# Kernel tuning notes

Hardware: AMD Instinct MI355X
Metric: run time of the kernel (lower is better)

Reference implementation:

```python
import jax, jax.numpy as jnp
import numpy as np

D_MODEL = 1024
NHEAD = 16
D_K = D_MODEL // NHEAD


def setup_inputs() -> dict:
    key = jax.random.key(0)
    ks = jax.random.split(key, 10)
    B, S = 2, 2048
    x = jax.random.normal(ks[0], (B, S, D_MODEL), dtype=jnp.float32)
    # sorted 1-D coordinate grid in [0,1], shape [S,1,1] so coords.shape[1]==1
    coords = jnp.sort(jax.random.uniform(ks[1], (S, 1, 1), dtype=jnp.float32), axis=0)
    sc = 1.0 / np.sqrt(D_MODEL)
    Wq = jax.random.normal(ks[2], (D_MODEL, D_MODEL), dtype=jnp.float32) * sc
    bq = jnp.zeros((D_MODEL,), jnp.float32)
    Wk = jax.random.normal(ks[3], (D_MODEL, D_MODEL), dtype=jnp.float32) * sc
    bk = jnp.zeros((D_MODEL,), jnp.float32)
    Wv = jax.random.normal(ks[4], (D_MODEL, D_MODEL), dtype=jnp.float32) * sc
    bv = jnp.zeros((D_MODEL,), jnp.float32)
    Wo = jax.random.normal(ks[5], (D_MODEL, D_MODEL), dtype=jnp.float32) * sc
    bo = jnp.zeros((D_MODEL,), jnp.float32)
    return {"x": x, "coords": coords, "Wq": Wq, "bq": bq, "Wk": Wk, "bk": bk,
            "Wv": Wv, "bv": bv, "Wo": Wo, "bo": bo}


def _split_heads(t):  # [B,S,D] -> [B,H,S,Dk]
    B, S, _ = t.shape
    return t.reshape(B, S, NHEAD, D_K).transpose(0, 2, 1, 3)


def reference(x, coords, Wq, bq, Wk, bk, Wv, bv, Wo, bo):
    B, S, _ = x.shape
    Q = _split_heads(x @ Wq.T + bq)
    K = _split_heads(x @ Wk.T + bk)
    V = _split_heads(x @ Wv.T + bv)

    scale = jnp.sqrt(jnp.float32(D_K))
    scores = jnp.einsum('bhld,bhsd->bhls', Q, K) / scale  # [B,H,S,S]

    # trapezoidal quadrature weights from coord grid: [S-1] -> broadcast shapes
    dc = jnp.abs(coords[1:] - coords[:-1]).reshape(1, 1, 1, S - 1)  # key-axis

    # custom trapezoidal softmax
    e = jnp.exp(scores - jnp.max(scores, axis=-1, keepdims=True))
    denom = jnp.sum(0.5 * dc * (e[..., 1:] + e[..., :-1]), axis=-1, keepdims=True)
    aw = e / denom  # [B,H,S,S]

    dcv = dc.reshape(1, 1, S - 1, 1)  # value-axis weighting
    o1 = jnp.einsum('bhls,bhsd->bhld', aw[..., 1:], dcv * V[:, :, 1:, :])
    o2 = jnp.einsum('bhls,bhsd->bhld', aw[..., :-1], dcv * V[:, :, :-1, :])
    out = 0.5 * (o1 + o2)  # [B,H,S,Dk]

    out = out.transpose(0, 2, 1, 3).reshape(B, S, D_MODEL)
    return out @ Wo.T + bo
```

## Files before the change

kernel.cpp:

```cpp
#include <hip/hip_runtime.h>

#define DM 1024
#define NHEAD 16
#define DK 64
#define QLD 3072

typedef short bf16x8 __attribute__((ext_vector_type(8)));
typedef float f32x4 __attribute__((ext_vector_type(4)));

__device__ __forceinline__ unsigned short f2bf(float f) {
  union { float f; unsigned u; } v; v.f = f;
  return (unsigned short)((v.u + 0x7fffu + ((v.u >> 16) & 1u)) >> 16);
}
__device__ __forceinline__ float bf2f(unsigned short h) {
  union { unsigned u; float f; } v; v.u = ((unsigned)h) << 16; return v.f;
}
__device__ __forceinline__ float fexp2(float x) {
  float r; asm("v_exp_f32 %0, %1" : "=v"(r) : "v"(x)); return r;
}

__device__ __forceinline__ void gld16(const void* g, void* l) {
  __builtin_amdgcn_global_load_lds((const __attribute__((address_space(1))) void*)g,
                                   (__attribute__((address_space(3))) void*)l, 16, 0, 0);
}

__device__ __forceinline__ int kappa(int p) {
  return (p & 32) + (((p & 7) >> 2) << 4) + (((p >> 3) & 3) << 2) + (p & 3);
}

__global__ void k_prep(const float* __restrict__ x, const float* __restrict__ Wq,
                       const float* __restrict__ Wk, const float* __restrict__ Wv,
                       const float* __restrict__ Wo, const float* __restrict__ bq,
                       const float* __restrict__ bk, const float* __restrict__ bv,
                       const float* __restrict__ coords,
                       unsigned short* __restrict__ xb, unsigned short* __restrict__ Wcat,
                       unsigned short* __restrict__ Wob, float* __restrict__ bcat,
                       float* __restrict__ tw, unsigned short* __restrict__ twb,
                       int M, int S, float QS) {
  const int nx = M * DM / 4;
  const int nw = DM * DM / 4;
  const int total = nx + 4 * nw;
  int gid = blockIdx.x * 256 + threadIdx.x;

  auto conv4 = [&](const float* src, unsigned short* dst, int idx, float sc) {
    float4 v = *(const float4*)(src + idx * 4);
    ushort4 o;
    o.x = f2bf(v.x * sc); o.y = f2bf(v.y * sc);
    o.z = f2bf(v.z * sc); o.w = f2bf(v.w * sc);
    *(ushort4*)(dst + idx * 4) = o;
  };

  if (gid < nx) { conv4(x, xb, gid, 1.0f); return; }
  if (gid < nx + nw) { conv4(Wq, Wcat, gid - nx, QS); return; }
  if (gid < nx + 2 * nw) { conv4(Wk, Wcat + DM * DM, gid - nx - nw, 1.0f); return; }
  if (gid < nx + 3 * nw) { conv4(Wv, Wcat + 2 * DM * DM, gid - nx - 2 * nw, 1.0f); return; }
  if (gid < total) { conv4(Wo, Wob, gid - nx - 3 * nw, 1.0f); return; }

  int r = gid - total;
  if (r < 3 * DM) {
    float v = (r < DM) ? bq[r] * QS : (r < 2 * DM ? bk[r - DM] : bv[r - 2 * DM]);
    bcat[r] = v;
    return;
  }
  r -= 3 * DM;
  if (r < S) {
    auto twval = [&](int k) {
      float a = (k > 0)     ? fabsf(coords[k] - coords[k - 1]) : 0.f;
      float b = (k < S - 1) ? fabsf(coords[k + 1] - coords[k]) : 0.f;
      return 0.5f * (a + b);
    };
    tw[r] = twval(r);
    int key = (r & ~63) + kappa(r & 63);
    twb[r] = f2bf(twval(key));
  }
}

#define BM 128
#define BN 128
#define BKK 64

template<int VFUSE>
__global__ __launch_bounds__(256)
void gemm_bt(const unsigned short* __restrict__ A, const unsigned short* __restrict__ B,
             const float* __restrict__ bias, void* __restrict__ C,
             int M, int N, int K, int ldc,
             const float* __restrict__ twp, unsigned short* __restrict__ Vt, int S) {
  __shared__ __align__(16) unsigned short smem[4][BM * BKK];
  const int tid = threadIdx.x;
  const int lane = tid & 63;
  const int wid = tid >> 6;
  const int rr = lane & 15, g = lane >> 4;
  const int nbn = N / BN;
  const int cpx = gridDim.x >> 3;
  const int bid = ((gridDim.x & 7) == 0) ? (blockIdx.x & 7) * cpx + (blockIdx.x >> 3)
                                         : blockIdx.x;
  const int bm = bid / nbn, bn = bid % nbn;
  const int wr = wid >> 1, wc = wid & 1;
  const int nkt = K / BKK;

  const unsigned short* Abase = A + (size_t)bm * BM * K;
  const unsigned short* Bbase = B + (size_t)bn * BN * K;

  auto stage = [&](int buf, int kt) {
#pragma unroll
    for (int j = 0; j < 4; ++j) {
      int o = j * 256 + tid;
      int row = o >> 3;
      int cb = ((o & 7) * 16) ^ ((row & 7) << 4);
      gld16((const char*)(Abase + (size_t)row * K + kt * BKK) + cb, &smem[buf][o * 8]);
      gld16((const char*)(Bbase + (size_t)row * K + kt * BKK) + cb, &smem[2 + buf][o * 8]);
    }
  };

  f32x4 acc[4][4] = {};
  stage(0, 0);
  int cur = 0;
  const int sw = (rr & 7) << 4;
  for (int kt = 0; kt < nkt; ++kt) {
    __syncthreads();
    if (kt + 1 < nkt) stage(cur ^ 1, kt + 1);
    const char* a0 = (const char*)&smem[cur][0];
    const char* b0 = (const char*)&smem[2 + cur][0];
#pragma unroll
    for (int kk = 0; kk < 2; ++kk) {
      const int co = (kk * 64 + g * 16);
      bf16x8 af[4], bfr[4];
#pragma unroll
      for (int m = 0; m < 4; ++m)
        af[m] = *(const bf16x8*)(a0 + (wr * 64 + m * 16 + rr) * 128 + (co ^ sw));
#pragma unroll
      for (int n = 0; n < 4; ++n)
        bfr[n] = *(const bf16x8*)(b0 + (wc * 64 + n * 16 + rr) * 128 + (co ^ sw));
      __builtin_amdgcn_s_setprio(1);
#pragma unroll
      for (int m = 0; m < 4; ++m)
#pragma unroll
        for (int n = 0; n < 4; ++n)
          acc[m][n] = __builtin_amdgcn_mfma_f32_16x16x32_bf16(af[m], bfr[n], acc[m][n], 0, 0, 0);
      __builtin_amdgcn_s_setprio(0);
    }
    cur ^= 1;
  }

  const int ccol0 = bn * BN + wc * 64;
  unsigned short* L = &smem[0][0];
  __syncthreads();
#pragma unroll
  for (int n = 0; n < 4; ++n) {
    const float bn_ = bias ? bias[ccol0 + n * 16 + rr] : 0.f;
#pragma unroll
    for (int m = 0; m < 4; ++m)
#pragma unroll
      for (int r = 0; r < 4; ++r)
        L[(wr * 64 + m * 16 + g * 4 + r) * 136 + wc * 64 + n * 16 + rr] =
            f2bf(acc[m][n][r] + bn_);
  }
  __syncthreads();
  if (VFUSE && bn >= (2 * DM) / BN) {
    const int tilesPerB = S / BM;
    const int bb = bm / tilesPerB;
    const int s0 = (bm % tilesPerB) * BM;
    const int vcol0 = bn * BN - 2 * DM;
    const int hh = tid >> 7;
    const int dd = (tid >> 1) & 63;
    const int stl = tid & 1;
    const int head = (vcol0 >> 6) + hh;
    const int lcol = hh * 64 + dd;
    unsigned short* vdst = Vt + ((size_t)(bb * NHEAD + head) * DK + dd) * S + s0 + stl * 64;
    const float* twg = twp + s0 + stl * 64;
    unsigned short tmp[8];
#pragma unroll
    for (int j8 = 0; j8 < 8; ++j8) {
#pragma unroll
      for (int j = 0; j < 8; ++j) {
        const int kl = kappa(j8 * 8 + j);
        tmp[j] = f2bf(bf2f(L[(stl * 64 + kl) * 136 + lcol]) * twg[kl]);
      }
      *(uint4*)&vdst[j8 * 8] = *(const uint4*)&tmp[0];
    }
  } else {
    unsigned short* Cb = (unsigned short*)C + (size_t)(bm * BM) * ldc + bn * BN;
#pragma unroll
    for (int i = 0; i < 8; ++i) {
      int o = i * 256 + tid;
      int row = o >> 4;
      int cc = (o & 15) * 8;
      uint4 v = *(const uint4*)&L[row * 136 + cc];
      *(uint4*)&Cb[(size_t)row * ldc + cc] = v;
    }
  }
}

#define WBM 64
__global__ __launch_bounds__(256)
void gemm_wo(const unsigned short* __restrict__ A, const unsigned short* __restrict__ B,
             const float* __restrict__ bias, float* __restrict__ C,
             int M, int N, int K, int ldc) {
  __shared__ __align__(16) unsigned short smem[6][WBM * BKK];
  const int tid = threadIdx.x;
  const int lane = tid & 63;
  const int wid = tid >> 6;
  const int rr = lane & 15, g = lane >> 4;
  const int nbn = N / BN;
  const int cpx = gridDim.x >> 3;
  const int bid = (blockIdx.x & 7) * cpx + (blockIdx.x >> 3);
  const int bm = bid / nbn, bn = bid % nbn;
  const int wr = wid >> 1, wc = wid & 1;
  const int nkt = K / BKK;

  const unsigned short* Abase = A + (size_t)bm * WBM * K;
  const unsigned short* Bbase = B + (size_t)bn * BN * K;

  auto stage = [&](int buf, int kt) {
    {
#pragma unroll
      for (int j = 0; j < 2; ++j) {
        int o = j * 256 + tid;
        int row = o >> 3;
        int cb = ((o & 7) * 16) ^ ((row & 7) << 4);
        gld16((const char*)(Abase + (size_t)row * K + kt * BKK) + cb, &smem[buf][o * 8]);
      }
    }
    {
#pragma unroll
      for (int j = 0; j < 4; ++j) {
        int o = j * 256 + tid;
        int row = o >> 3;
        int cb = ((o & 7) * 16) ^ ((row & 7) << 4);
        gld16((const char*)(Bbase + (size_t)row * K + kt * BKK) + cb, &smem[2 + buf * 2][o * 8]);
      }
    }
  };

  f32x4 acc[2][4] = {};
  stage(0, 0);
  int cur = 0;
  const int sw = (rr & 7) << 4;
  for (int kt = 0; kt < nkt; ++kt) {
    __syncthreads();
    if (kt + 1 < nkt) stage(cur ^ 1, kt + 1);
    const char* a0 = (const char*)&smem[cur][0];
    const char* b0 = (const char*)&smem[2 + cur * 2][0];
#pragma unroll
    for (int kk = 0; kk < 2; ++kk) {
      const int co = (kk * 64 + g * 16);
      bf16x8 af[2], bfr[4];
#pragma unroll
      for (int m = 0; m < 2; ++m)
        af[m] = *(const bf16x8*)(a0 + (wr * 32 + m * 16 + rr) * 128 + (co ^ sw));
#pragma unroll
      for (int n = 0; n < 4; ++n)
        bfr[n] = *(const bf16x8*)(b0 + (wc * 64 + n * 16 + rr) * 128 + (co ^ sw));
      __builtin_amdgcn_s_setprio(1);
#pragma unroll
      for (int m = 0; m < 2; ++m)
#pragma unroll
        for (int n = 0; n < 4; ++n)
          acc[m][n] = __builtin_amdgcn_mfma_f32_16x16x32_bf16(af[m], bfr[n], acc[m][n], 0, 0, 0);
      __builtin_amdgcn_s_setprio(0);
    }
    cur ^= 1;
  }

  float* Lf = (float*)&smem[0][0];
  __syncthreads();
#pragma unroll
  for (int n = 0; n < 4; ++n) {
    const float bn_ = bias[bn * BN + wc * 64 + n * 16 + rr];
#pragma unroll
    for (int m = 0; m < 2; ++m)
#pragma unroll
      for (int r = 0; r < 4; ++r)
        Lf[(wr * 32 + m * 16 + g * 4 + r) * 132 + wc * 64 + n * 16 + rr] =
            acc[m][n][r] + bn_;
  }
  __syncthreads();
  float* Cb = C + (size_t)(bm * WBM) * ldc + bn * BN;
#pragma unroll
  for (int i = 0; i < 8; ++i) {
    int o = i * 256 + tid;
    int row = o >> 5;
    int cc = (o & 31) * 4;
    float4 v = *(const float4*)&Lf[row * 132 + cc];
    *(float4*)&Cb[(size_t)row * ldc + cc] = v;
  }
}

__global__ __launch_bounds__(256)
void k_attn(const unsigned short* __restrict__ QKV, const unsigned short* __restrict__ Vt,
            const unsigned short* __restrict__ twb, unsigned short* __restrict__ O, int S) {
  __shared__ __align__(16) unsigned short sK[2][128 * 64];
  __shared__ __align__(16) unsigned short sV[2][2][64 * 64];
  const int tid = threadIdx.x, lane = tid & 63, wid = tid >> 6;
  const int rr = lane & 15, g = lane >> 4;
  const int nqt = S / 128;
  const int cpx = gridDim.x >> 3;
  const int swz = (blockIdx.x & 7) * cpx + (blockIdx.x >> 3);
  const int qt = swz % nqt;
  const int bh = swz / nqt;
  const int h = bh & (NHEAD - 1), b = bh / NHEAD;

  const unsigned short* Qbase = QKV + ((size_t)b * S + qt * 128 + wid * 32) * QLD + h * DK;
  const unsigned short* Kbase = QKV + (size_t)b * S * QLD + DM + h * DK;
  const unsigned short* Vbase = Vt + (size_t)bh * DK * S;

  bf16x8 aq[2][2];
#pragma unroll
  for (int qm = 0; qm < 2; ++qm) {
    aq[qm][0] = *(const bf16x8*)&Qbase[(size_t)(qm * 16 + rr) * QLD + g * 8];
    aq[qm][1] = *(const bf16x8*)&Qbase[(size_t)(qm * 16 + rr) * QLD + 32 + g * 8];
  }

  f32x4 acc[2][5] = {};
  const f32x4 z0 = {};

  auto stage = [&](int buf, int kt) {
#pragma unroll
    for (int j = 0; j < 4; ++j) {
      int o = j * 256 + tid;
      int row = o >> 3;
      int cb = ((o & 7) * 16) ^ ((row & 7) << 4);
      gld16((const char*)(Kbase + (size_t)(kt * 128 + row) * QLD) + cb, &sK[buf][o * 8]);
    }
#pragma unroll
    for (int j = 0; j < 4; ++j) {
      int o = j * 256 + tid;
      int half_ = o >> 9;
      int r = o & 511;
      int row = r >> 3;
      int cb = ((r & 7) * 16) ^ ((row & 7) << 4);
      gld16((const char*)(Vbase + (size_t)row * S + kt * 128 + half_ * 64) + cb,
            &sV[buf][0][o * 8]);
    }
  };

  stage(0, 0);
  int cur = 0;
  const int nkt = S / 128;
  const int swr = (rr & 7) << 4;
  for (int kt = 0; kt < nkt; ++kt) {
    __syncthreads();
    if (kt + 1 < nkt) stage(cur ^ 1, kt + 1);

#pragma unroll
    for (int half = 0; half < 2; ++half) {
      bf16x8 kA[4][2];
#pragma unroll
      for (int f = 0; f < 4; ++f) {
        const int row = half * 64 + f * 16 + rr;
        kA[f][0] = *(const bf16x8*)((const char*)&sK[cur][row * 64] + ((g * 16) ^ swr));
        kA[f][1] = *(const bf16x8*)((const char*)&sK[cur][row * 64] + ((64 + g * 16) ^ swr));
      }
      bf16x8 vB[2][4];
#pragma unroll
      for (int kk = 0; kk < 2; ++kk)
#pragma unroll
        for (int n = 0; n < 4; ++n) {
          const int vrow = n * 16 + rr;
          const int cb = (kk * 64 + g * 16) ^ ((vrow & 7) << 4);
          vB[kk][n] = *(const bf16x8*)((const char*)&sV[cur][half][vrow * 64] + cb);
        }
      bf16x8 tw0 = *(const bf16x8*)&twb[kt * 128 + half * 64 + g * 8];
      bf16x8 tw1 = *(const bf16x8*)&twb[kt * 128 + half * 64 + 32 + g * 8];

      f32x4 s[2][4];
      __builtin_amdgcn_s_setprio(1);
#pragma unroll
      for (int f = 0; f < 4; ++f)
#pragma unroll
        for (int qm = 0; qm < 2; ++qm) {
          f32x4 z = __builtin_amdgcn_mfma_f32_16x16x32_bf16(kA[f][0], aq[qm][0], z0, 0, 0, 0);
          s[qm][f] = __builtin_amdgcn_mfma_f32_16x16x32_bf16(kA[f][1], aq[qm][1], z, 0, 0, 0);
        }
      __builtin_amdgcn_s_setprio(0);

#pragma unroll
      for (int qm = 0; qm < 2; ++qm)
#pragma unroll
        for (int f = 0; f < 4; ++f)
#pragma unroll
          for (int r = 0; r < 4; ++r)
            s[qm][f][r] = fexp2(s[qm][f][r]);

      bf16x8 pa[2][2];
#pragma unroll
      for (int qm = 0; qm < 2; ++qm)
#pragma unroll
        for (int kk = 0; kk < 2; ++kk) {
          union { bf16x8 v; unsigned u[4]; } pk;
          asm("v_cvt_pk_bf16_f32 %0, %1, %2" : "=v"(pk.u[0]) : "v"(s[qm][2*kk][0]),   "v"(s[qm][2*kk][1]));
          asm("v_cvt_pk_bf16_f32 %0, %1, %2" : "=v"(pk.u[1]) : "v"(s[qm][2*kk][2]),   "v"(s[qm][2*kk][3]));
          asm("v_cvt_pk_bf16_f32 %0, %1, %2" : "=v"(pk.u[2]) : "v"(s[qm][2*kk+1][0]), "v"(s[qm][2*kk+1][1]));
          asm("v_cvt_pk_bf16_f32 %0, %1, %2" : "=v"(pk.u[3]) : "v"(s[qm][2*kk+1][2]), "v"(s[qm][2*kk+1][3]));
          pa[qm][kk] = pk.v;
        }

      __builtin_amdgcn_s_setprio(1);
#pragma unroll
      for (int kk = 0; kk < 2; ++kk) {
#pragma unroll
        for (int n = 0; n < 4; ++n)
#pragma unroll
          for (int qm = 0; qm < 2; ++qm)
            acc[qm][n] = __builtin_amdgcn_mfma_f32_16x16x32_bf16(pa[qm][kk], vB[kk][n], acc[qm][n], 0, 0, 0);
#pragma unroll
        for (int qm = 0; qm < 2; ++qm)
          acc[qm][4] = __builtin_amdgcn_mfma_f32_16x16x32_bf16(pa[qm][kk], kk ? tw1 : tw0, acc[qm][4], 0, 0, 0);
      }
      __builtin_amdgcn_s_setprio(0);
    }
    cur ^= 1;
  }

  unsigned short* L = &sK[0][0];
  __syncthreads();
#pragma unroll
  for (int qm = 0; qm < 2; ++qm)
#pragma unroll
    for (int n = 0; n < 4; ++n)
#pragma unroll
      for (int r = 0; r < 4; ++r)
        L[(wid * 32 + qm * 16 + g * 4 + r) * 72 + n * 16 + rr] =
            f2bf(acc[qm][n][r] / acc[qm][4][r]);
  __syncthreads();
  unsigned short* Ob = O + ((size_t)b * S + qt * 128) * DM + h * DK;
#pragma unroll
  for (int i = 0; i < 4; ++i) {
    int o = i * 256 + tid;
    int row = o >> 3;
    int c = (o & 7) * 8;
    uint4 v = *(const uint4*)&L[row * 72 + c];
    *(uint4*)&Ob[(size_t)row * DM + c] = v;
  }
}

extern "C" void kernel_launch(void* const* d_in, const int* in_sizes, int n_in,
                              void* d_out, int out_size, void* d_ws, size_t ws_size,
                              hipStream_t stream) {
  const float* x      = (const float*)d_in[0];
  const float* coords = (const float*)d_in[1];
  const float* Wq = (const float*)d_in[2];
  const float* bq = (const float*)d_in[3];
  const float* Wk = (const float*)d_in[4];
  const float* bk = (const float*)d_in[5];
  const float* Wv = (const float*)d_in[6];
  const float* bv = (const float*)d_in[7];
  const float* Wo = (const float*)d_in[8];
  const float* bo = (const float*)d_in[9];

  const int S = in_sizes[1];
  const int B = in_sizes[0] / (S * DM);
  const int M = B * S;
  const float QS = 0.18033688011112042f;

  char* w = (char*)d_ws;
  size_t off = 0;
  unsigned short* xb   = (unsigned short*)(w + off); off += (size_t)M * DM * 2;
  unsigned short* Wcat = (unsigned short*)(w + off); off += (size_t)3 * DM * DM * 2;
  unsigned short* Wob  = (unsigned short*)(w + off); off += (size_t)DM * DM * 2;
  unsigned short* QKVb = (unsigned short*)(w + off); off += (size_t)M * QLD * 2;
  unsigned short* Vtb  = (unsigned short*)(w + off); off += (size_t)M * DM * 2;
  float* tw  = (float*)(w + off); off += (size_t)S * 4;
  unsigned short* twb = (unsigned short*)(w + off); off += (size_t)S * 2;
  float* bcat = (float*)(w + off); off += (size_t)3 * DM * 4;
  unsigned short* Ob = xb;
  (void)ws_size; (void)n_in; (void)out_size;

  {
    int nx = M * DM / 4, nw = DM * DM / 4;
    int total = nx + 4 * nw;
    int tail = 3 * DM + S;
    int gridp = total / 256 + (tail + 255) / 256;
    k_prep<<<gridp, 256, 0, stream>>>(x, Wq, Wk, Wv, Wo, bq, bk, bv, coords,
                                      xb, Wcat, Wob, bcat, tw, twb, M, S, QS);
  }

  gemm_bt<1><<<(M / BM) * (3 * DM / BN), 256, 0, stream>>>(
      xb, Wcat, bcat, QKVb, M, 3 * DM, DM, QLD, tw, Vtb, S);

  k_attn<<<B * NHEAD * (S / 128), 256, 0, stream>>>(QKVb, Vtb, twb, Ob, S);

  gemm_wo<<<(M / WBM) * (DM / BN), 256, 0, stream>>>(Ob, Wob, bo, (float*)d_out, M, DM, DM, DM);
}
```

Measured before the change: 107.3 us.

## Fuse fp32-to-bf16 weight conversion into GEMM B-tile staging

Weight conversion to bf16 is removed from the prep kernel. Instead each GEMM block loads fp32 weight tiles into registers, prefetching one k-step ahead, then converts and writes them to swizzled LDS after the MFMA loop. This saves a full pass that reads the weights and writes a bf16 copy. In exchange, every M-tile re-reads the fp32 weights at twice the bytes, register pressure rises, and a launch_bounds occupancy hint of 2 is added.

New measurement: 147.5 us. 37.6% more time.

```diff
diff --git a/kernel.cpp b/kernel.cpp
--- a/kernel.cpp
+++ b/kernel.cpp
@@ -24,39 +24,35 @@
                                    (__attribute__((address_space(3))) void*)l, 16, 0, 0);
 }
 
+__device__ __forceinline__ uint4 pack8(float4 a, float4 b, float sc) {
+  uint4 r;
+  r.x = (unsigned)f2bf(a.x * sc) | ((unsigned)f2bf(a.y * sc) << 16);
+  r.y = (unsigned)f2bf(a.z * sc) | ((unsigned)f2bf(a.w * sc) << 16);
+  r.z = (unsigned)f2bf(b.x * sc) | ((unsigned)f2bf(b.y * sc) << 16);
+  r.w = (unsigned)f2bf(b.z * sc) | ((unsigned)f2bf(b.w * sc) << 16);
+  return r;
+}
+
 __device__ __forceinline__ int kappa(int p) {
   return (p & 32) + (((p & 7) >> 2) << 4) + (((p >> 3) & 3) << 2) + (p & 3);
 }
 
-__global__ void k_prep(const float* __restrict__ x, const float* __restrict__ Wq,
-                       const float* __restrict__ Wk, const float* __restrict__ Wv,
-                       const float* __restrict__ Wo, const float* __restrict__ bq,
+__global__ void k_prep(const float* __restrict__ x, const float* __restrict__ bq,
                        const float* __restrict__ bk, const float* __restrict__ bv,
                        const float* __restrict__ coords,
-                       unsigned short* __restrict__ xb, unsigned short* __restrict__ Wcat,
-                       unsigned short* __restrict__ Wob, float* __restrict__ bcat,
+                       unsigned short* __restrict__ xb, float* __restrict__ bcat,
                        float* __restrict__ tw, unsigned short* __restrict__ twb,
                        int M, int S, float QS) {
-  const int nx = M * DM / 4;
-  const int nw = DM * DM / 4;
-  const int total = nx + 4 * nw;
+  const int nx8 = M * DM / 8;
   int gid = blockIdx.x * 256 + threadIdx.x;
 
-  auto conv4 = [&](const float* src, unsigned short* dst, int idx, float sc) {
-    float4 v = *(const float4*)(src + idx * 4);
-    ushort4 o;
-    o.x = f2bf(v.x * sc); o.y = f2bf(v.y * sc);
-    o.z = f2bf(v.z * sc); o.w = f2bf(v.w * sc);
-    *(ushort4*)(dst + idx * 4) = o;
-  };
-
-  if (gid < nx) { conv4(x, xb, gid, 1.0f); return; }
-  if (gid < nx + nw) { conv4(Wq, Wcat, gid - nx, QS); return; }
-  if (gid < nx + 2 * nw) { conv4(Wk, Wcat + DM * DM, gid - nx - nw, 1.0f); return; }
-  if (gid < nx + 3 * nw) { conv4(Wv, Wcat + 2 * DM * DM, gid - nx - 2 * nw, 1.0f); return; }
-  if (gid < total) { conv4(Wo, Wob, gid - nx - 3 * nw, 1.0f); return; }
-
-  int r = gid - total;
+  if (gid < nx8) {
+    float4 a = *(const float4*)(x + gid * 8);
+    float4 b = *(const float4*)(x + gid * 8 + 4);
+    *(uint4*)(xb + gid * 8) = pack8(a, b, 1.0f);
+    return;
+  }
+  int r = gid - nx8;
   if (r < 3 * DM) {
     float v = (r < DM) ? bq[r] * QS : (r < 2 * DM ? bk[r - DM] : bv[r - 2 * DM]);
     bcat[r] = v;
@@ -79,9 +75,10 @@
 #define BN 128
 #define BKK 64
 
-template<int VFUSE>
-__global__ __launch_bounds__(256)
-void gemm_bt(const unsigned short* __restrict__ A, const unsigned short* __restrict__ B,
+__global__ __launch_bounds__(256, 2)
+void gemm_bt(const unsigned short* __restrict__ A,
+             const float* __restrict__ Wq, const float* __restrict__ Wk,
+             const float* __restrict__ Wv, float QS,
              const float* __restrict__ bias, void* __restrict__ C,
              int M, int N, int K, int ldc,
              const float* __restrict__ twp, unsigned short* __restrict__ Vt, int S) {
@@ -92,33 +89,58 @@
   const int rr = lane & 15, g = lane >> 4;
   const int nbn = N / BN;
   const int cpx = gridDim.x >> 3;
-  const int bid = ((gridDim.x & 7) == 0) ? (blockIdx.x & 7) * cpx + (blockIdx.x >> 3)
-                                         : blockIdx.x;
+  const int bid = (blockIdx.x & 7) * cpx + (blockIdx.x >> 3);
   const int bm = bid / nbn, bn = bid % nbn;
   const int wr = wid >> 1, wc = wid & 1;
   const int nkt = K / BKK;
 
   const unsigned short* Abase = A + (size_t)bm * BM * K;
-  const unsigned short* Bbase = B + (size_t)bn * BN * K;
-
-  auto stage = [&](int buf, int kt) {
+  const int sel = bn >> 3;
+  const float* Wsel = (sel == 0) ? Wq : ((sel == 1) ? Wk : Wv);
+  const float wsc = (sel == 0) ? QS : 1.0f;
+  const int brow0 = bn * BN - sel * 1024;
+
+  auto stageA = [&](int buf, int kt) {
 #pragma unroll
     for (int j = 0; j < 4; ++j) {
       int o = j * 256 + tid;
       int row = o >> 3;
       int cb = ((o & 7) * 16) ^ ((row & 7) << 4);
       gld16((const char*)(Abase + (size_t)row * K + kt * BKK) + cb, &smem[buf][o * 8]);
-      gld16((const char*)(Bbase + (size_t)row * K + kt * BKK) + cb, &smem[2 + buf][o * 8]);
+    }
+  };
+
+  float4 vb0[4], vb1[4];
+  auto issueB = [&](int kt) {
+#pragma unroll
+    for (int j = 0; j < 4; ++j) {
+      int o = j * 256 + tid;
+      int row = o >> 3;
+      int ce = (o & 7) * 8;
+      const float* src = Wsel + (size_t)(brow0 + row) * K + kt * BKK + ce;
+      vb0[j] = *(const float4*)src;
+      vb1[j] = *(const float4*)(src + 4);
+    }
+  };
+  auto writeB = [&](int buf) {
+#pragma unroll
+    for (int j = 0; j < 4; ++j) {
+      int o = j * 256 + tid;
+      int row = o >> 3;
+      int cb = ((o & 7) * 16) ^ ((row & 7) << 4);
+      *(uint4*)((char*)&smem[2 + buf][0] + row * 128 + cb) = pack8(vb0[j], vb1[j], wsc);
     }
   };
 
   f32x4 acc[4][4] = {};
-  stage(0, 0);
+  stageA(0, 0);
+  issueB(0);
+  writeB(0);
   int cur = 0;
   const int sw = (rr & 7) << 4;
   for (int kt = 0; kt < nkt; ++kt) {
     __syncthreads();
-    if (kt + 1 < nkt) stage(cur ^ 1, kt + 1);
+    if (kt + 1 < nkt) { stageA(cur ^ 1, kt + 1); issueB(kt + 1); }
     const char* a0 = (const char*)&smem[cur][0];
     const char* b0 = (const char*)&smem[2 + cur][0];
 #pragma unroll
@@ -139,6 +161,7 @@
           acc[m][n] = __builtin_amdgcn_mfma_f32_16x16x32_bf16(af[m], bfr[n], acc[m][n], 0, 0, 0);
       __builtin_amdgcn_s_setprio(0);
     }
+    if (kt + 1 < nkt) writeB(cur ^ 1);
     cur ^= 1;
   }
 
@@ -156,7 +179,7 @@
             f2bf(acc[m][n][r] + bn_);
   }
   __syncthreads();
-  if (VFUSE && bn >= (2 * DM) / BN) {
+  if (bn >= (2 * DM) / BN) {
     const int tilesPerB = S / BM;
     const int bb = bm / tilesPerB;
     const int s0 = (bm % tilesPerB) * BM;
@@ -192,8 +215,8 @@
 }
 
 #define WBM 64
-__global__ __launch_bounds__(256)
-void gemm_wo(const unsigned short* __restrict__ A, const unsigned short* __restrict__ B,
+__global__ __launch_bounds__(256, 2)
+void gemm_wo(const unsigned short* __restrict__ A, const float* __restrict__ Wo,
              const float* __restrict__ bias, float* __restrict__ C,
              int M, int N, int K, int ldc) {
   __shared__ __align__(16) unsigned short smem[6][WBM * BKK];
@@ -209,36 +232,48 @@
   const int nkt = K / BKK;
 
   const unsigned short* Abase = A + (size_t)bm * WBM * K;
-  const unsigned short* Bbase = B + (size_t)bn * BN * K;
-
-  auto stage = [&](int buf, int kt) {
-    {
-#pragma unroll
-      for (int j = 0; j < 2; ++j) {
-        int o = j * 256 + tid;
-        int row = o >> 3;
-        int cb = ((o & 7) * 16) ^ ((row & 7) << 4);
-        gld16((const char*)(Abase + (size_t)row * K + kt * BKK) + cb, &smem[buf][o * 8]);
-      }
-    }
-    {
-#pragma unroll
-      for (int j = 0; j < 4; ++j) {
-        int o = j * 256 + tid;
-        int row = o >> 3;
-        int cb = ((o & 7) * 16) ^ ((row & 7) << 4);
-        gld16((const char*)(Bbase + (size_t)row * K + kt * BKK) + cb, &smem[2 + buf * 2][o * 8]);
-      }
+
+  auto stageA = [&](int buf, int kt) {
+#pragma unroll
+    for (int j = 0; j < 2; ++j) {
+      int o = j * 256 + tid;
+      int row = o >> 3;
+      int cb = ((o & 7) * 16) ^ ((row & 7) << 4);
+      gld16((const char*)(Abase + (size_t)row * K + kt * BKK) + cb, &smem[buf][o * 8]);
+    }
+  };
+
+  float4 vb0[4], vb1[4];
+  auto issueB = [&](int kt) {
+#pragma unroll
+    for (int j = 0; j < 4; ++j) {
+      int o = j * 256 + tid;
+      int row = o >> 3;
+      int ce = (o & 7) * 8;
+      const float* src = Wo + (size_t)(bn * BN + row) * K + kt * BKK + ce;
+      vb0[j] = *(const float4*)src;
+      vb1[j] = *(const float4*)(src + 4);
+    }
+  };
+  auto writeB = [&](int buf) {
+#pragma unroll
+    for (int j = 0; j < 4; ++j) {
+      int o = j * 256 + tid;
+      int row = o >> 3;
+      int cb = ((o & 7) * 16) ^ ((row & 7) << 4);
+      *(uint4*)((char*)&smem[2 + buf * 2][0] + row * 128 + cb) = pack8(vb0[j], vb1[j], 1.0f);
     }
   };
 
   f32x4 acc[2][4] = {};
-  stage(0, 0);
+  stageA(0, 0);
+  issueB(0);
+  writeB(0);
   int cur = 0;
   const int sw = (rr & 7) << 4;
   for (int kt = 0; kt < nkt; ++kt) {
     __syncthreads();
-    if (kt + 1 < nkt) stage(cur ^ 1, kt + 1);
+    if (kt + 1 < nkt) { stageA(cur ^ 1, kt + 1); issueB(kt + 1); }
     const char* a0 = (const char*)&smem[cur][0];
     const char* b0 = (const char*)&smem[2 + cur * 2][0];
 #pragma unroll
@@ -259,6 +294,7 @@
           acc[m][n] = __builtin_amdgcn_mfma_f32_16x16x32_bf16(af[m], bfr[n], acc[m][n], 0, 0, 0);
       __builtin_amdgcn_s_setprio(0);
     }
+    if (kt + 1 < nkt) writeB(cur ^ 1);
     cur ^= 1;
   }
 
@@ -456,8 +492,6 @@
   char* w = (char*)d_ws;
   size_t off = 0;
   unsigned short* xb   = (unsigned short*)(w + off); off += (size_t)M * DM * 2;
-  unsigned short* Wcat = (unsigned short*)(w + off); off += (size_t)3 * DM * DM * 2;
-  unsigned short* Wob  = (unsigned short*)(w + off); off += (size_t)DM * DM * 2;
   unsigned short* QKVb = (unsigned short*)(w + off); off += (size_t)M * QLD * 2;
   unsigned short* Vtb  = (unsigned short*)(w + off); off += (size_t)M * DM * 2;
   float* tw  = (float*)(w + off); off += (size_t)S * 4;
@@ -467,18 +501,16 @@
   (void)ws_size; (void)n_in; (void)out_size;
 
   {
-    int nx = M * DM / 4, nw = DM * DM / 4;
-    int total = nx + 4 * nw;
+    int nx8 = M * DM / 8;
     int tail = 3 * DM + S;
-    int gridp = total / 256 + (tail + 255) / 256;
-    k_prep<<<gridp, 256, 0, stream>>>(x, Wq, Wk, Wv, Wo, bq, bk, bv, coords,
-                                      xb, Wcat, Wob, bcat, tw, twb, M, S, QS);
-  }
-
-  gemm_bt<1><<<(M / BM) * (3 * DM / BN), 256, 0, stream>>>(
-      xb, Wcat, bcat, QKVb, M, 3 * DM, DM, QLD, tw, Vtb, S);
+    int gridp = nx8 / 256 + (tail + 255) / 256;
+    k_prep<<<gridp, 256, 0, stream>>>(x, bq, bk, bv, coords, xb, bcat, tw, twb, M, S, QS);
+  }
+
+  gemm_bt<<<(M / BM) * (3 * DM / BN), 256, 0, stream>>>(
+      xb, Wq, Wk, Wv, QS, bcat, QKVb, M, 3 * DM, DM, QLD, tw, Vtb, S);
 
   k_attn<<<B * NHEAD * (S / 128), 256, 0, stream>>>(QKVb, Vtb, twb, Ob, S);
 
-  gemm_wo<<<(M / WBM) * (DM / BN), 256, 0, stream>>>(Ob, Wob, bo, (float*)d_out, M, DM, DM, DM);
-}
+  gemm_wo<<<(M / WBM) * (DM / BN), 256, 0, stream>>>(Ob, Wo, bo, (float*)d_out, M, DM, DM, DM);
+}
```
